# Performance work log

Measured on AMD Instinct MI355X. Metric: run time of the kernel, lower is better.

## Reference

```python
import jax, jax.numpy as jnp
import numpy as np

VOXEL_RES = 4
CLASSES = 40


def setup_inputs() -> dict:
    key = jax.random.key(0)
    kx, kw, kb = jax.random.split(key, 3)
    B, N = 64, 100000
    x = jax.random.normal(kx, (B, N, 3), dtype=jnp.float32)
    F = VOXEL_RES ** 3
    bound = 1.0 / np.sqrt(F)  # torch Linear default init range
    W = jax.random.uniform(kw, (CLASSES, F), minval=-bound, maxval=bound, dtype=jnp.float32)
    b = jax.random.uniform(kb, (CLASSES,), minval=-bound, maxval=bound, dtype=jnp.float32)
    return {"x": x, "W": W, "b": b}


def reference(x, W, b):
    # x: (B, N, 3). Faithful to torch.histogramdd(bins=R): the histogram range
    # per dimension is [min, max] of the data; the last bin is right-inclusive.
    B, N, _ = x.shape
    R = VOXEL_RES
    mn = jnp.min(x, axis=1, keepdims=True)  # (B, 1, 3)
    mx = jnp.max(x, axis=1, keepdims=True)  # (B, 1, 3)
    # bin index = floor((v - min) / (max - min) * R), clipped so v == max -> R-1
    idx = jnp.floor((x - mn) / (mx - mn) * R).astype(jnp.int32)
    idx = jnp.clip(idx, 0, R - 1)  # (B, N, 3)
    flat = idx[..., 0] * R * R + idx[..., 1] * R + idx[..., 2]  # (B, N)
    flat = flat + (jnp.arange(B, dtype=jnp.int32) * (R ** 3))[:, None]
    counts = jax.ops.segment_sum(
        jnp.ones((B * N,), dtype=x.dtype), flat.reshape(-1), num_segments=B * R ** 3
    ).reshape(B, R ** 3)
    counts = counts / N  # fraction of points per voxel
    class_outputs = counts @ W.T + b  # (B, classes)
    return class_outputs
```

## Files before the change

kernel.cpp:

```cpp
#include <hip/hip_runtime.h>

#define VR 4
#define NVOX 64
#define NCLS 40
#define NB 64
#define NPTS 100000
#define BPB 16
#define G_PER_B (NPTS / 4)
#define F4_PER_B (NPTS * 3 / 4)
#define STRIDE_G (BPB * 256)
#define FLT_BIG 3.402823466e38f

__global__ __launch_bounds__(256) void minmax_k(const float4* __restrict__ x,
                                                float* __restrict__ pmin,
                                                float* __restrict__ pmax) {
    const int b = blockIdx.x / BPB;
    const int sub = blockIdx.x % BPB;
    const float4* xb = x + (size_t)b * F4_PER_B;

    float mn0 = FLT_BIG, mn1 = FLT_BIG, mn2 = FLT_BIG;
    float mx0 = -FLT_BIG, mx1 = -FLT_BIG, mx2 = -FLT_BIG;

    for (int base = sub * 256; base < G_PER_B; base += STRIDE_G) {
        int g = base + (int)threadIdx.x;
        bool valid = g < G_PER_B;
        int gc = valid ? g : (G_PER_B - 1);
        float4 a = xb[3 * gc];
        float4 c = xb[3 * gc + 1];
        float4 e = xb[3 * gc + 2];
        if (valid) {
            mn0 = fminf(mn0, fminf(fminf(a.x, a.w), fminf(c.z, e.y)));
            mx0 = fmaxf(mx0, fmaxf(fmaxf(a.x, a.w), fmaxf(c.z, e.y)));
            mn1 = fminf(mn1, fminf(fminf(a.y, c.x), fminf(c.w, e.z)));
            mx1 = fmaxf(mx1, fmaxf(fmaxf(a.y, c.x), fmaxf(c.w, e.z)));
            mn2 = fminf(mn2, fminf(fminf(a.z, c.y), fminf(e.x, e.w)));
            mx2 = fmaxf(mx2, fmaxf(fmaxf(a.z, c.y), fmaxf(e.x, e.w)));
        }
    }

    #pragma unroll
    for (int off = 32; off > 0; off >>= 1) {
        mn0 = fminf(mn0, __shfl_down(mn0, off, 64));
        mn1 = fminf(mn1, __shfl_down(mn1, off, 64));
        mn2 = fminf(mn2, __shfl_down(mn2, off, 64));
        mx0 = fmaxf(mx0, __shfl_down(mx0, off, 64));
        mx1 = fmaxf(mx1, __shfl_down(mx1, off, 64));
        mx2 = fmaxf(mx2, __shfl_down(mx2, off, 64));
    }

    __shared__ float smn[4][3], smx[4][3];
    const int lane = threadIdx.x & 63;
    const int wv = threadIdx.x >> 6;
    if (lane == 0) {
        smn[wv][0] = mn0; smn[wv][1] = mn1; smn[wv][2] = mn2;
        smx[wv][0] = mx0; smx[wv][1] = mx1; smx[wv][2] = mx2;
    }
    __syncthreads();
    if (threadIdx.x < 3) {
        const int d = threadIdx.x;
        float a = smn[0][d], z = smx[0][d];
        #pragma unroll
        for (int w = 1; w < 4; w++) {
            a = fminf(a, smn[w][d]);
            z = fmaxf(z, smx[w][d]);
        }
        pmin[(b * BPB + sub) * 3 + d] = a;
        pmax[(b * BPB + sub) * 3 + d] = z;
    }
}

__device__ __forceinline__ int bin1(float v, float mn, float s4) {
    int i = (int)((v - mn) * s4);
    return i > (VR - 1) ? (VR - 1) : i;
}

__device__ __forceinline__ void tally(int v, unsigned long long vm,
                                      const unsigned long long* ns,
                                      unsigned& cnt) {
    unsigned long long b0 = __ballot(v & 1);
    unsigned long long b1 = __ballot(v & 2);
    unsigned long long b2 = __ballot(v & 4);
    unsigned long long b3 = __ballot(v & 8);
    unsigned long long b4 = __ballot(v & 16);
    unsigned long long b5 = __ballot(v & 32);
    unsigned long long m = vm & (b0 ^ ns[0]) & (b1 ^ ns[1]) & (b2 ^ ns[2])
                              & (b3 ^ ns[3]) & (b4 ^ ns[4]) & (b5 ^ ns[5]);
    cnt += (unsigned)__popcll(m);
}

__global__ __launch_bounds__(256) void hist_k(const float4* __restrict__ x,
                                              const float* __restrict__ pmin,
                                              const float* __restrict__ pmax,
                                              unsigned* __restrict__ phist) {
    const int b = blockIdx.x / BPB;
    const int sub = blockIdx.x % BPB;
    const float4* xb = x + (size_t)b * F4_PER_B;
    const int lane = threadIdx.x & 63;
    const int wv = threadIdx.x >> 6;

    __shared__ float smm[6];
    if (threadIdx.x < 6) {
        int d = threadIdx.x % 3;
        bool isMax = threadIdx.x >= 3;
        float r = isMax ? -FLT_BIG : FLT_BIG;
        for (int s = 0; s < BPB; s++) {
            float v = isMax ? pmax[(b * BPB + s) * 3 + d]
                            : pmin[(b * BPB + s) * 3 + d];
            r = isMax ? fmaxf(r, v) : fminf(r, v);
        }
        smm[threadIdx.x] = r;
    }
    __syncthreads();
    const float mn_0 = smm[0], mn_1 = smm[1], mn_2 = smm[2];
    const float s4_0 = (float)VR / (smm[3] - smm[0]);
    const float s4_1 = (float)VR / (smm[4] - smm[1]);
    const float s4_2 = (float)VR / (smm[5] - smm[2]);

    unsigned long long ns[6];
    #pragma unroll
    for (int k = 0; k < 6; k++)
        ns[k] = ((lane >> k) & 1) ? 0ull : ~0ull;

    unsigned cnt = 0;
    for (int base = sub * 256; base < G_PER_B; base += STRIDE_G) {
        int g = base + (int)threadIdx.x;
        bool valid = g < G_PER_B;
        int gc = valid ? g : (G_PER_B - 1);
        float4 a = xb[3 * gc];
        float4 c = xb[3 * gc + 1];
        float4 e = xb[3 * gc + 2];
        unsigned long long vm = __ballot(valid);
        int v0 = bin1(a.x, mn_0, s4_0) * 16 + bin1(a.y, mn_1, s4_1) * 4 + bin1(a.z, mn_2, s4_2);
        int v1 = bin1(a.w, mn_0, s4_0) * 16 + bin1(c.x, mn_1, s4_1) * 4 + bin1(c.y, mn_2, s4_2);
        int v2 = bin1(c.z, mn_0, s4_0) * 16 + bin1(c.w, mn_1, s4_1) * 4 + bin1(e.x, mn_2, s4_2);
        int v3 = bin1(e.y, mn_0, s4_0) * 16 + bin1(e.z, mn_1, s4_1) * 4 + bin1(e.w, mn_2, s4_2);
        tally(v0, vm, ns, cnt);
        tally(v1, vm, ns, cnt);
        tally(v2, vm, ns, cnt);
        tally(v3, vm, ns, cnt);
    }

    __shared__ unsigned swh[4][NVOX];
    swh[wv][lane] = cnt;
    __syncthreads();
    if (threadIdx.x < NVOX) {
        phist[(b * BPB + sub) * NVOX + threadIdx.x] =
            swh[0][threadIdx.x] + swh[1][threadIdx.x] +
            swh[2][threadIdx.x] + swh[3][threadIdx.x];
    }
}

__global__ __launch_bounds__(256) void gemv_k(const unsigned* __restrict__ phist,
                                              const float* __restrict__ W,
                                              const float* __restrict__ bias,
                                              float* __restrict__ out) {
    const int b = blockIdx.x;
    __shared__ float fh[NVOX];
    __shared__ float sW[NCLS * NVOX];

    if (threadIdx.x < NVOX) {
        unsigned s = 0;
        for (int p = 0; p < BPB; p++)
            s += phist[(b * BPB + p) * NVOX + threadIdx.x];
        fh[threadIdx.x] = (float)s * (1.0f / (float)NPTS);
    }
    for (int i = threadIdx.x; i < NCLS * NVOX; i += 256)
        sW[i] = W[i];
    __syncthreads();

    if (threadIdx.x < NCLS) {
        const int c = threadIdx.x;
        float acc = 0.f;
        #pragma unroll
        for (int f = 0; f < NVOX; f++)
            acc += fh[f] * sW[c * NVOX + f];
        out[b * NCLS + c] = acc + bias[c];
    }
}

extern "C" void kernel_launch(void* const* d_in, const int* in_sizes, int n_in,
                              void* d_out, int out_size, void* d_ws, size_t ws_size,
                              hipStream_t stream) {
    const float* x = (const float*)d_in[0];
    const float* W = (const float*)d_in[1];
    const float* bias = (const float*)d_in[2];
    float* out = (float*)d_out;

    float* pmin = (float*)d_ws;
    float* pmax = pmin + NB * BPB * 3;
    unsigned* phist = (unsigned*)(pmax + NB * BPB * 3);

    minmax_k<<<NB * BPB, 256, 0, stream>>>((const float4*)x, pmin, pmax);
    hist_k<<<NB * BPB, 256, 0, stream>>>((const float4*)x, pmin, pmax, phist);
    gemv_k<<<NB, 256, 0, stream>>>(phist, W, bias, out);
}
```

Measured before the change: 125.0 us.

## Fuse minmax, histogram and GEMV into one cooperative kernel with grid syncs

Replaces the three launches with one cooperative kernel of 1024 blocks that uses grid-wide syncs between the min/max, histogram and GEMV phases. Each block's second pass over its slice of x may hit in cache, since the same block reads the same addresses again. The loops are split into fully unrolled bounds-free iterations plus a tail. This trades launch gaps for the cost of two grid barriers and requires all 1024 blocks to be co-resident.

```diff
diff --git a/kernel.cpp b/kernel.cpp
--- a/kernel.cpp
+++ b/kernel.cpp
@@ -1,4 +1,7 @@
 #include <hip/hip_runtime.h>
+#include <hip/hip_cooperative_groups.h>
+
+namespace cg = cooperative_groups;
 
 #define VR 4
 #define NVOX 64
@@ -6,36 +9,74 @@
 #define NB 64
 #define NPTS 100000
 #define BPB 16
+#define NBLK (NB * BPB)
 #define G_PER_B (NPTS / 4)
 #define F4_PER_B (NPTS * 3 / 4)
 #define STRIDE_G (BPB * 256)
+#define FULL_ITERS (G_PER_B / STRIDE_G)
+#define TAIL_G (G_PER_B - FULL_ITERS * STRIDE_G)
 #define FLT_BIG 3.402823466e38f
 
-__global__ __launch_bounds__(256) void minmax_k(const float4* __restrict__ x,
-                                                float* __restrict__ pmin,
-                                                float* __restrict__ pmax) {
+__device__ __forceinline__ int bin1(float v, float mn, float s4) {
+    int i = (int)((v - mn) * s4);
+    return i > (VR - 1) ? (VR - 1) : i;
+}
+
+__device__ __forceinline__ unsigned long long vox_mask(
+        int v, const unsigned long long* ns) {
+    return (__ballot(v & 1)  ^ ns[0]) & (__ballot(v & 2)  ^ ns[1])
+         & (__ballot(v & 4)  ^ ns[2]) & (__ballot(v & 8)  ^ ns[3])
+         & (__ballot(v & 16) ^ ns[4]) & (__ballot(v & 32) ^ ns[5]);
+}
+
+__global__ __launch_bounds__(256, 4) void fused_k(
+        const float4* __restrict__ x, const float* __restrict__ W,
+        const float* __restrict__ bias, float* __restrict__ out,
+        float* __restrict__ pmin, float* __restrict__ pmax,
+        unsigned* __restrict__ phist) {
     const int b = blockIdx.x / BPB;
     const int sub = blockIdx.x % BPB;
     const float4* xb = x + (size_t)b * F4_PER_B;
+    const int lane = threadIdx.x & 63;
+    const int wv = threadIdx.x >> 6;
+    const int t0 = sub * 256 + (int)threadIdx.x;
+
+    __shared__ float sW[NCLS * NVOX];
+    __shared__ float smn[4][3], smx[4][3];
+    __shared__ float smm[6];
+    __shared__ unsigned swh[4][NVOX];
+    __shared__ float fh[NVOX];
+
+    if (blockIdx.x < NB)
+        for (int i = threadIdx.x; i < NCLS * NVOX; i += 256)
+            sW[i] = W[i];
 
     float mn0 = FLT_BIG, mn1 = FLT_BIG, mn2 = FLT_BIG;
     float mx0 = -FLT_BIG, mx1 = -FLT_BIG, mx2 = -FLT_BIG;
-
-    for (int base = sub * 256; base < G_PER_B; base += STRIDE_G) {
-        int g = base + (int)threadIdx.x;
-        bool valid = g < G_PER_B;
-        int gc = valid ? g : (G_PER_B - 1);
-        float4 a = xb[3 * gc];
-        float4 c = xb[3 * gc + 1];
-        float4 e = xb[3 * gc + 2];
-        if (valid) {
-            mn0 = fminf(mn0, fminf(fminf(a.x, a.w), fminf(c.z, e.y)));
-            mx0 = fmaxf(mx0, fmaxf(fmaxf(a.x, a.w), fmaxf(c.z, e.y)));
-            mn1 = fminf(mn1, fminf(fminf(a.y, c.x), fminf(c.w, e.z)));
-            mx1 = fmaxf(mx1, fmaxf(fmaxf(a.y, c.x), fmaxf(c.w, e.z)));
-            mn2 = fminf(mn2, fminf(fminf(a.z, c.y), fminf(e.x, e.w)));
-            mx2 = fmaxf(mx2, fmaxf(fmaxf(a.z, c.y), fmaxf(e.x, e.w)));
-        }
+    #pragma unroll
+    for (int k = 0; k < FULL_ITERS; k++) {
+        const int g = t0 + k * STRIDE_G;
+        float4 a = xb[3 * g];
+        float4 c = xb[3 * g + 1];
+        float4 e = xb[3 * g + 2];
+        mn0 = fminf(mn0, fminf(fminf(a.x, a.w), fminf(c.z, e.y)));
+        mx0 = fmaxf(mx0, fmaxf(fmaxf(a.x, a.w), fmaxf(c.z, e.y)));
+        mn1 = fminf(mn1, fminf(fminf(a.y, c.x), fminf(c.w, e.z)));
+        mx1 = fmaxf(mx1, fmaxf(fmaxf(a.y, c.x), fmaxf(c.w, e.z)));
+        mn2 = fminf(mn2, fminf(fminf(a.z, c.y), fminf(e.x, e.w)));
+        mx2 = fmaxf(mx2, fmaxf(fmaxf(a.z, c.y), fmaxf(e.x, e.w)));
+    }
+    if (sub * 256 < TAIL_G && t0 < TAIL_G) {
+        const int g = FULL_ITERS * STRIDE_G + t0;
+        float4 a = xb[3 * g];
+        float4 c = xb[3 * g + 1];
+        float4 e = xb[3 * g + 2];
+        mn0 = fminf(mn0, fminf(fminf(a.x, a.w), fminf(c.z, e.y)));
+        mx0 = fmaxf(mx0, fmaxf(fmaxf(a.x, a.w), fmaxf(c.z, e.y)));
+        mn1 = fminf(mn1, fminf(fminf(a.y, c.x), fminf(c.w, e.z)));
+        mx1 = fmaxf(mx1, fmaxf(fmaxf(a.y, c.x), fmaxf(c.w, e.z)));
+        mn2 = fminf(mn2, fminf(fminf(a.z, c.y), fminf(e.x, e.w)));
+        mx2 = fmaxf(mx2, fmaxf(fmaxf(a.z, c.y), fmaxf(e.x, e.w)));
     }
 
     #pragma unroll
@@ -47,10 +88,6 @@
         mx1 = fmaxf(mx1, __shfl_down(mx1, off, 64));
         mx2 = fmaxf(mx2, __shfl_down(mx2, off, 64));
     }
-
-    __shared__ float smn[4][3], smx[4][3];
-    const int lane = threadIdx.x & 63;
-    const int wv = threadIdx.x >> 6;
     if (lane == 0) {
         smn[wv][0] = mn0; smn[wv][1] = mn1; smn[wv][2] = mn2;
         smx[wv][0] = mx0; smx[wv][1] = mx1; smx[wv][2] = mx2;
@@ -67,41 +104,12 @@
         pmin[(b * BPB + sub) * 3 + d] = a;
         pmax[(b * BPB + sub) * 3 + d] = z;
     }
-}
-
-__device__ __forceinline__ int bin1(float v, float mn, float s4) {
-    int i = (int)((v - mn) * s4);
-    return i > (VR - 1) ? (VR - 1) : i;
-}
-
-__device__ __forceinline__ void tally(int v, unsigned long long vm,
-                                      const unsigned long long* ns,
-                                      unsigned& cnt) {
-    unsigned long long b0 = __ballot(v & 1);
-    unsigned long long b1 = __ballot(v & 2);
-    unsigned long long b2 = __ballot(v & 4);
-    unsigned long long b3 = __ballot(v & 8);
-    unsigned long long b4 = __ballot(v & 16);
-    unsigned long long b5 = __ballot(v & 32);
-    unsigned long long m = vm & (b0 ^ ns[0]) & (b1 ^ ns[1]) & (b2 ^ ns[2])
-                              & (b3 ^ ns[3]) & (b4 ^ ns[4]) & (b5 ^ ns[5]);
-    cnt += (unsigned)__popcll(m);
-}
-
-__global__ __launch_bounds__(256) void hist_k(const float4* __restrict__ x,
-                                              const float* __restrict__ pmin,
-                                              const float* __restrict__ pmax,
-                                              unsigned* __restrict__ phist) {
-    const int b = blockIdx.x / BPB;
-    const int sub = blockIdx.x % BPB;
-    const float4* xb = x + (size_t)b * F4_PER_B;
-    const int lane = threadIdx.x & 63;
-    const int wv = threadIdx.x >> 6;
-
-    __shared__ float smm[6];
+
+    cg::this_grid().sync();
+
     if (threadIdx.x < 6) {
-        int d = threadIdx.x % 3;
-        bool isMax = threadIdx.x >= 3;
+        const int d = threadIdx.x % 3;
+        const bool isMax = threadIdx.x >= 3;
         float r = isMax ? -FLT_BIG : FLT_BIG;
         for (int s = 0; s < BPB; s++) {
             float v = isMax ? pmax[(b * BPB + s) * 3 + d]
@@ -111,10 +119,10 @@
         smm[threadIdx.x] = r;
     }
     __syncthreads();
-    const float mn_0 = smm[0], mn_1 = smm[1], mn_2 = smm[2];
-    const float s4_0 = (float)VR / (smm[3] - smm[0]);
-    const float s4_1 = (float)VR / (smm[4] - smm[1]);
-    const float s4_2 = (float)VR / (smm[5] - smm[2]);
+    const float bn0 = smm[0], bn1 = smm[1], bn2 = smm[2];
+    const float s40 = (float)VR / (smm[3] - smm[0]);
+    const float s41 = (float)VR / (smm[4] - smm[1]);
+    const float s42 = (float)VR / (smm[5] - smm[2]);
 
     unsigned long long ns[6];
     #pragma unroll
@@ -122,75 +130,86 @@
         ns[k] = ((lane >> k) & 1) ? 0ull : ~0ull;
 
     unsigned cnt = 0;
-    for (int base = sub * 256; base < G_PER_B; base += STRIDE_G) {
-        int g = base + (int)threadIdx.x;
-        bool valid = g < G_PER_B;
-        int gc = valid ? g : (G_PER_B - 1);
-        float4 a = xb[3 * gc];
-        float4 c = xb[3 * gc + 1];
-        float4 e = xb[3 * gc + 2];
-        unsigned long long vm = __ballot(valid);
-        int v0 = bin1(a.x, mn_0, s4_0) * 16 + bin1(a.y, mn_1, s4_1) * 4 + bin1(a.z, mn_2, s4_2);
-        int v1 = bin1(a.w, mn_0, s4_0) * 16 + bin1(c.x, mn_1, s4_1) * 4 + bin1(c.y, mn_2, s4_2);
-        int v2 = bin1(c.z, mn_0, s4_0) * 16 + bin1(c.w, mn_1, s4_1) * 4 + bin1(e.x, mn_2, s4_2);
-        int v3 = bin1(e.y, mn_0, s4_0) * 16 + bin1(e.z, mn_1, s4_1) * 4 + bin1(e.w, mn_2, s4_2);
-        tally(v0, vm, ns, cnt);
-        tally(v1, vm, ns, cnt);
-        tally(v2, vm, ns, cnt);
-        tally(v3, vm, ns, cnt);
-    }
-
-    __shared__ unsigned swh[4][NVOX];
+    #pragma unroll 2
+    for (int k = 0; k < FULL_ITERS; k++) {
+        const int g = t0 + k * STRIDE_G;
+        float4 a = xb[3 * g];
+        float4 c = xb[3 * g + 1];
+        float4 e = xb[3 * g + 2];
+        int v0 = bin1(a.x, bn0, s40) * 16 + bin1(a.y, bn1, s41) * 4 + bin1(a.z, bn2, s42);
+        int v1 = bin1(a.w, bn0, s40) * 16 + bin1(c.x, bn1, s41) * 4 + bin1(c.y, bn2, s42);
+        int v2 = bin1(c.z, bn0, s40) * 16 + bin1(c.w, bn1, s41) * 4 + bin1(e.x, bn2, s42);
+        int v3 = bin1(e.y, bn0, s40) * 16 + bin1(e.z, bn1, s41) * 4 + bin1(e.w, bn2, s42);
+        cnt += (unsigned)__popcll(vox_mask(v0, ns));
+        cnt += (unsigned)__popcll(vox_mask(v1, ns));
+        cnt += (unsigned)__popcll(vox_mask(v2, ns));
+        cnt += (unsigned)__popcll(vox_mask(v3, ns));
+    }
+    if (sub * 256 < TAIL_G) {
+        const bool valid = t0 < TAIL_G;
+        const unsigned long long vm = __ballot(valid);
+        const int g = FULL_ITERS * STRIDE_G + (valid ? t0 : 0);
+        float4 a = xb[3 * g];
+        float4 c = xb[3 * g + 1];
+        float4 e = xb[3 * g + 2];
+        int v0 = bin1(a.x, bn0, s40) * 16 + bin1(a.y, bn1, s41) * 4 + bin1(a.z, bn2, s42);
+        int v1 = bin1(a.w, bn0, s40) * 16 + bin1(c.x, bn1, s41) * 4 + bin1(c.y, bn2, s42);
+        int v2 = bin1(c.z, bn0, s40) * 16 + bin1(c.w, bn1, s41) * 4 + bin1(e.x, bn2, s42);
+        int v3 = bin1(e.y, bn0, s40) * 16 + bin1(e.z, bn1, s41) * 4 + bin1(e.w, bn2, s42);
+        cnt += (unsigned)__popcll(vm & vox_mask(v0, ns));
+        cnt += (unsigned)__popcll(vm & vox_mask(v1, ns));
+        cnt += (unsigned)__popcll(vm & vox_mask(v2, ns));
+        cnt += (unsigned)__popcll(vm & vox_mask(v3, ns));
+    }
+
     swh[wv][lane] = cnt;
     __syncthreads();
-    if (threadIdx.x < NVOX) {
+    if (threadIdx.x < NVOX)
         phist[(b * BPB + sub) * NVOX + threadIdx.x] =
             swh[0][threadIdx.x] + swh[1][threadIdx.x] +
             swh[2][threadIdx.x] + swh[3][threadIdx.x];
-    }
-}
-
-__global__ __launch_bounds__(256) void gemv_k(const unsigned* __restrict__ phist,
-                                              const float* __restrict__ W,
-                                              const float* __restrict__ bias,
-                                              float* __restrict__ out) {
-    const int b = blockIdx.x;
-    __shared__ float fh[NVOX];
-    __shared__ float sW[NCLS * NVOX];
-
-    if (threadIdx.x < NVOX) {
+
+    cg::this_grid().sync();
+
+    if (blockIdx.x >= NB) return;
+    {
+        const int vox = threadIdx.x & 63;
+        const int part = threadIdx.x >> 6;
         unsigned s = 0;
-        for (int p = 0; p < BPB; p++)
-            s += phist[(b * BPB + p) * NVOX + threadIdx.x];
-        fh[threadIdx.x] = (float)s * (1.0f / (float)NPTS);
-    }
-    for (int i = threadIdx.x; i < NCLS * NVOX; i += 256)
-        sW[i] = W[i];
-    __syncthreads();
-
+        #pragma unroll
+        for (int p = 0; p < 4; p++)
+            s += phist[(blockIdx.x * BPB + part * 4 + p) * NVOX + vox];
+        swh[part][vox] = s;
+    }
+    __syncthreads();
+    if (threadIdx.x < NVOX)
+        fh[threadIdx.x] = (float)(swh[0][threadIdx.x] + swh[1][threadIdx.x] +
+                                  swh[2][threadIdx.x] + swh[3][threadIdx.x])
+                          * (1.0f / (float)NPTS);
+    __syncthreads();
     if (threadIdx.x < NCLS) {
-        const int c = threadIdx.x;
         float acc = 0.f;
         #pragma unroll
         for (int f = 0; f < NVOX; f++)
-            acc += fh[f] * sW[c * NVOX + f];
-        out[b * NCLS + c] = acc + bias[c];
+            acc += fh[f] * sW[threadIdx.x * NVOX + f];
+        out[blockIdx.x * NCLS + threadIdx.x] = acc + bias[threadIdx.x];
     }
 }
 
 extern "C" void kernel_launch(void* const* d_in, const int* in_sizes, int n_in,
                               void* d_out, int out_size, void* d_ws, size_t ws_size,
                               hipStream_t stream) {
-    const float* x = (const float*)d_in[0];
+    const float4* x = (const float4*)d_in[0];
     const float* W = (const float*)d_in[1];
     const float* bias = (const float*)d_in[2];
     float* out = (float*)d_out;
 
     float* pmin = (float*)d_ws;
-    float* pmax = pmin + NB * BPB * 3;
-    unsigned* phist = (unsigned*)(pmax + NB * BPB * 3);
-
-    minmax_k<<<NB * BPB, 256, 0, stream>>>((const float4*)x, pmin, pmax);
-    hist_k<<<NB * BPB, 256, 0, stream>>>((const float4*)x, pmin, pmax, phist);
-    gemv_k<<<NB, 256, 0, stream>>>(phist, W, bias, out);
-}
+    float* pmax = pmin + NBLK * 3;
+    unsigned* phist = (unsigned*)(pmax + NBLK * 3);
+
+    void* args[] = {(void*)&x, (void*)&W, (void*)&bias, (void*)&out,
+                    (void*)&pmin, (void*)&pmax, (void*)&phist};
+    hipLaunchCooperativeKernel((const void*)fused_k, dim3(NBLK), dim3(256),
+                               args, 0, stream);
+}
```

After: 362.9 us. +190.4%, slower.
